# Kernel optimization log

Hardware: AMD Instinct MI355X
Metric: run time of the kernel (lower is better)

Reference implementation:

```python
import jax, jax.numpy as jnp
import numpy as np

SOFT_WINDOW_SIGMA = 4.0
QUERY_DIM = 512
B, T_DEC, T_ENC, D_V = 32, 2048, 2048, 512


def setup_inputs() -> dict:
    key = jax.random.key(0)
    kq, kk, kv = jax.random.split(key, 3)
    queries = jax.random.normal(kq, (B, T_DEC, QUERY_DIM), dtype=jnp.float32)
    keys = jax.random.normal(kk, (B, T_ENC, QUERY_DIM), dtype=jnp.float32)
    values = jax.random.normal(kv, (B, T_ENC, D_V), dtype=jnp.float32)
    return {"queries": queries, "keys": keys, "values": values}


def reference(queries, keys, values):
    # scores[b,i,j] = <q_i, k_j> ; [B, T_dec, T_enc]
    scale = 1.0 / np.sqrt(queries.shape[-1])
    scores = jnp.einsum('bid,bjd->bij', queries, keys)
    t_dec, t_enc = scores.shape[1], scores.shape[2]
    # soft window bias: (1 / (2*sigma^2)) * (i - (T_dec/T_enc) * j)
    i = jnp.arange(t_dec, dtype=jnp.float32)[:, None]
    j = jnp.arange(t_enc, dtype=jnp.float32)[None, :]
    soft_window = (1.0 / (2.0 * SOFT_WINDOW_SIGMA ** 2)) * (i - (t_dec / t_enc) * j)
    scores = jax.nn.softmax(scores * scale - soft_window, axis=2)
    summaries = jnp.einsum('bij,bjv->biv', scores, values)
    return (summaries, scores)
```

## Files before the change

kernel.cpp:

```cpp
#include <hip/hip_runtime.h>
#include <cstdint>
#include <cstddef>


#define NB 32
#define TD 2048
#define TE 2048
#define DQ 512
#define DV 512

static constexpr float SCALE = 0.04419417382415922f;
static constexpr float WBIAS = 0.03125f;

typedef __bf16 bf16x8 __attribute__((ext_vector_type(8)));
typedef float f32x4 __attribute__((ext_vector_type(4)));

__device__ __forceinline__ unsigned short f2bf(float x) {
  unsigned int u = __float_as_uint(x);
  u = (u + 0x7fffu + ((u >> 16) & 1u)) >> 16;
  return (unsigned short)u;
}

__device__ __forceinline__ void gload_lds16(const void* g, void* l) {
  __builtin_amdgcn_global_load_lds(
      (const __attribute__((address_space(1))) void*)g,
      (__attribute__((address_space(3))) void*)l, 16, 0, 0);
}

__global__ __launch_bounds__(256) void k_cvt(const float4* __restrict__ src,
                                             ushort4* __restrict__ dst) {
  int i = blockIdx.x * 256 + threadIdx.x;
  float4 v = src[i];
  dst[i] = make_ushort4(f2bf(v.x), f2bf(v.y), f2bf(v.z), f2bf(v.w));
}

__global__ __launch_bounds__(256) void k_vtrans(const float* __restrict__ V,
                                                unsigned short* __restrict__ Vt) {
  __shared__ float t[32 * 33];
  int b = blockIdx.z, j0 = blockIdx.y * 32, v0 = blockIdx.x * 32;
  int tid = threadIdx.x;
  int r = tid >> 3, c4 = (tid & 7) * 4;
  float4 in = *(const float4*)(V + ((size_t)b * TE + j0 + r) * DV + v0 + c4);
  t[r * 33 + c4 + 0] = in.x;
  t[r * 33 + c4 + 1] = in.y;
  t[r * 33 + c4 + 2] = in.z;
  t[r * 33 + c4 + 3] = in.w;
  __syncthreads();
  ushort4 o = make_ushort4(f2bf(t[(c4 + 0) * 33 + r]), f2bf(t[(c4 + 1) * 33 + r]),
                           f2bf(t[(c4 + 2) * 33 + r]), f2bf(t[(c4 + 3) * 33 + r]));
  *(ushort4*)(Vt + ((size_t)b * DV + v0 + r) * TE + j0 + c4) = o;
}

__global__ __launch_bounds__(256) void k_gemm1(const unsigned short* __restrict__ Qb,
                                               const unsigned short* __restrict__ Kb,
                                               float* __restrict__ Sc) {
  __shared__ __align__(16) unsigned short As[128 * 32];
  __shared__ __align__(16) unsigned short Bs[128 * 32];
  int bid = blockIdx.x;
  int xcd = bid & 7, slot = bid >> 3;
  int b = xcd + 8 * (slot >> 8);
  int tile = slot & 255;
  int it = tile >> 4, jt = tile & 15;

  int tid = threadIdx.x, w = tid >> 6, l = tid & 63;
  int lr = l >> 2, lc = (l & 3) * 8;
  int lm = l & 15, quad = l >> 4;
  int wr = (w >> 1) * 64, wc = (w & 1) * 64;

  const size_t qbase = ((size_t)b * TD + (size_t)it * 128) * DQ;
  const size_t kbase = ((size_t)b * TE + (size_t)jt * 128) * DQ;

  f32x4 acc[4][4];
  f32x4 zero = {0.f, 0.f, 0.f, 0.f};
  for (int mi = 0; mi < 4; ++mi)
    for (int ni = 0; ni < 4; ++ni) acc[mi][ni] = zero;

  for (int k0 = 0; k0 < DQ; k0 += 32) {
    for (int t = 0; t < 2; ++t) {
      int rg = (w * 2 + t) * 16;
      gload_lds16(Qb + qbase + (size_t)(rg + lr) * DQ + k0 + lc, &As[rg * 32]);
      gload_lds16(Kb + kbase + (size_t)(rg + lr) * DQ + k0 + lc, &Bs[rg * 32]);
    }
    __syncthreads();
    bf16x8 af[4], bfr[4];
    for (int mi = 0; mi < 4; ++mi)
      af[mi] = *(const bf16x8*)&As[(wr + mi * 16 + lm) * 32 + quad * 8];
    for (int ni = 0; ni < 4; ++ni)
      bfr[ni] = *(const bf16x8*)&Bs[(wc + ni * 16 + lm) * 32 + quad * 8];
    for (int mi = 0; mi < 4; ++mi)
      for (int ni = 0; ni < 4; ++ni)
        acc[mi][ni] = __builtin_amdgcn_mfma_f32_16x16x32_bf16(af[mi], bfr[ni],
                                                              acc[mi][ni], 0, 0, 0);
    __syncthreads();
  }

  for (int mi = 0; mi < 4; ++mi) {
    int ib = it * 128 + wr + mi * 16 + quad * 4;
    for (int ni = 0; ni < 4; ++ni) {
      int j = jt * 128 + wc + ni * 16 + lm;
      float* op = Sc + ((size_t)b * TD + ib) * TE + j;
      for (int r = 0; r < 4; ++r) {
        float lg = acc[mi][ni][r] * SCALE - (float)(ib + r - j) * WBIAS;
        op[(size_t)r * TE] = lg;
      }
    }
  }
}

__global__ __launch_bounds__(256) void k_softmax(float* __restrict__ Sc) {
  int w = threadIdx.x >> 6, l = threadIdx.x & 63;
  size_t row = (size_t)blockIdx.x * 4 + w;
  float4* p = (float4*)(Sc + row * TE);
  float4 v[8];
  float m = -3.0e38f;
  for (int t = 0; t < 8; ++t) {
    v[t] = p[l + 64 * t];
    m = fmaxf(m, fmaxf(fmaxf(v[t].x, v[t].y), fmaxf(v[t].z, v[t].w)));
  }
  for (int off = 32; off; off >>= 1) m = fmaxf(m, __shfl_xor(m, off));
  float s = 0.f;
  for (int t = 0; t < 8; ++t) {
    v[t].x = __expf(v[t].x - m);
    v[t].y = __expf(v[t].y - m);
    v[t].z = __expf(v[t].z - m);
    v[t].w = __expf(v[t].w - m);
    s += (v[t].x + v[t].y) + (v[t].z + v[t].w);
  }
  for (int off = 32; off; off >>= 1) s += __shfl_xor(s, off);
  float inv = 1.0f / s;
  for (int t = 0; t < 8; ++t) {
    v[t].x *= inv; v[t].y *= inv; v[t].z *= inv; v[t].w *= inv;
    p[l + 64 * t] = v[t];
  }
}

__global__ __launch_bounds__(256) void k_gemm2(const float* __restrict__ Sc,
                                               const unsigned short* __restrict__ Vt,
                                               float* __restrict__ O) {
  __shared__ __align__(16) unsigned short As[64 * 32];
  __shared__ __align__(16) unsigned short Bs[512 * 32];
  int bid = blockIdx.x;
  int xcd = bid & 7, slot = bid >> 3;
  int b = xcd + 8 * (slot >> 5);
  int it = slot & 31;
  int i0 = it * 64;

  int tid = threadIdx.x, w = tid >> 6, l = tid & 63;
  int lm = l & 15, quad = l >> 4;
  int lr = l >> 2, lc = (l & 3) * 8;
  int arow = tid >> 2, acg = (tid & 3) * 8;
  const float* ap = Sc + ((size_t)b * TD + i0 + arow) * TE + acg;

  f32x4 acc[4][8];
  f32x4 zero = {0.f, 0.f, 0.f, 0.f};
  for (int mi = 0; mi < 4; ++mi)
    for (int ni = 0; ni < 8; ++ni) acc[mi][ni] = zero;

  for (int k0 = 0; k0 < TE; k0 += 32) {
    float4 f0 = *(const float4*)(ap + k0);
    float4 f1 = *(const float4*)(ap + k0 + 4);
    *(ushort4*)&As[arow * 32 + acg] =
        make_ushort4(f2bf(f0.x), f2bf(f0.y), f2bf(f0.z), f2bf(f0.w));
    *(ushort4*)&As[arow * 32 + acg + 4] =
        make_ushort4(f2bf(f1.x), f2bf(f1.y), f2bf(f1.z), f2bf(f1.w));
    for (int q = 0; q < 8; ++q) {
      int vr = (w * 8 + q) * 16;
      gload_lds16(Vt + ((size_t)b * DV + vr + lr) * TE + k0 + lc, &Bs[vr * 32]);
    }
    __syncthreads();
    bf16x8 af[4];
    for (int mi = 0; mi < 4; ++mi)
      af[mi] = *(const bf16x8*)&As[(mi * 16 + lm) * 32 + quad * 8];
    for (int ni = 0; ni < 8; ++ni) {
      bf16x8 bfr = *(const bf16x8*)&Bs[(w * 128 + ni * 16 + lm) * 32 + quad * 8];
      for (int mi = 0; mi < 4; ++mi)
        acc[mi][ni] = __builtin_amdgcn_mfma_f32_16x16x32_bf16(af[mi], bfr,
                                                              acc[mi][ni], 0, 0, 0);
    }
    __syncthreads();
  }

  for (int mi = 0; mi < 4; ++mi) {
    int ib = i0 + mi * 16 + quad * 4;
    for (int ni = 0; ni < 8; ++ni) {
      int vc = w * 128 + ni * 16 + lm;
      float* op = O + ((size_t)b * TD + ib) * DV + vc;
      for (int r = 0; r < 4; ++r) op[(size_t)r * DV] = acc[mi][ni][r];
    }
  }
}

extern "C" void kernel_launch(void* const* d_in, const int* in_sizes, int n_in,
                              void* d_out, int out_size, void* d_ws, size_t ws_size,
                              hipStream_t stream) {
  const float* Q = (const float*)d_in[0];
  const float* K = (const float*)d_in[1];
  const float* V = (const float*)d_in[2];
  float* out = (float*)d_out;
  float* O = out;
  float* Sc = out + (size_t)NB * TD * DV;

  unsigned short* qb = (unsigned short*)d_ws;
  unsigned short* kb = qb + (size_t)NB * TD * DQ;
  unsigned short* vt = kb + (size_t)NB * TE * DQ;

  k_cvt<<<32768, 256, 0, stream>>>((const float4*)Q, (ushort4*)qb);
  k_cvt<<<32768, 256, 0, stream>>>((const float4*)K, (ushort4*)kb);
  k_vtrans<<<dim3(16, 64, 32), 256, 0, stream>>>(V, vt);
  k_gemm1<<<8192, 256, 0, stream>>>(qb, kb, Sc);
  k_softmax<<<16384, 256, 0, stream>>>(Sc);
  k_gemm2<<<1024, 256, 0, stream>>>(Sc, vt, O);
}
```

Baseline: 1.569 ms.

## Fuse softmax into GEMM epilogues via partial row max/sum statistics

The standalone softmax kernel is removed. The first GEMM epilogue now computes per-row partial max and sum-of-exp over each 64-column slice and stores them in the output buffer as scratch. The second GEMM merges these partials, normalizes the scores on the fly, writes the probabilities back and feeds them to the MFMA. This drops one full read pass over the large score matrix and one kernel launch. In exchange it adds extra exp work and cross-lane shuffles in both GEMMs and relies on the output buffer as temporary storage. The two Q/K conversion launches are also merged into a single kernel.

```diff
diff --git a/kernel.cpp b/kernel.cpp
--- a/kernel.cpp
+++ b/kernel.cpp
@@ -27,11 +27,21 @@
       (__attribute__((address_space(3))) void*)l, 16, 0, 0);
 }
 
-__global__ __launch_bounds__(256) void k_cvt(const float4* __restrict__ src,
-                                             ushort4* __restrict__ dst) {
-  int i = blockIdx.x * 256 + threadIdx.x;
-  float4 v = src[i];
-  dst[i] = make_ushort4(f2bf(v.x), f2bf(v.y), f2bf(v.z), f2bf(v.w));
+__global__ __launch_bounds__(256) void k_cvt2(const float4* __restrict__ Q,
+                                              ushort4* __restrict__ Qb,
+                                              const float4* __restrict__ K,
+                                              ushort4* __restrict__ Kb) {
+  int bid = blockIdx.x;
+  const float4* s;
+  ushort4* d;
+  int i;
+  if (bid < 32768) {
+    s = Q; d = Qb; i = bid * 256 + threadIdx.x;
+  } else {
+    s = K; d = Kb; i = (bid - 32768) * 256 + threadIdx.x;
+  }
+  float4 v = s[i];
+  d[i] = make_ushort4(f2bf(v.x), f2bf(v.y), f2bf(v.z), f2bf(v.w));
 }
 
 __global__ __launch_bounds__(256) void k_vtrans(const float* __restrict__ V,
@@ -53,7 +63,8 @@
 
 __global__ __launch_bounds__(256) void k_gemm1(const unsigned short* __restrict__ Qb,
                                                const unsigned short* __restrict__ Kb,
-                                               float* __restrict__ Sc) {
+                                               float* __restrict__ Sc,
+                                               float* __restrict__ St) {
   __shared__ __align__(16) unsigned short As[128 * 32];
   __shared__ __align__(16) unsigned short Bs[128 * 32];
   int bid = blockIdx.x;
@@ -96,47 +107,49 @@
 
   for (int mi = 0; mi < 4; ++mi) {
     int ib = it * 128 + wr + mi * 16 + quad * 4;
+    float lg[4][4];
+#pragma unroll
     for (int ni = 0; ni < 4; ++ni) {
       int j = jt * 128 + wc + ni * 16 + lm;
       float* op = Sc + ((size_t)b * TD + ib) * TE + j;
+#pragma unroll
       for (int r = 0; r < 4; ++r) {
-        float lg = acc[mi][ni][r] * SCALE - (float)(ib + r - j) * WBIAS;
-        op[(size_t)r * TE] = lg;
+        float v = acc[mi][ni][r] * SCALE - (float)(ib + r - j) * WBIAS;
+        lg[ni][r] = v;
+        op[(size_t)r * TE] = v;
       }
     }
-  }
-}
-
-__global__ __launch_bounds__(256) void k_softmax(float* __restrict__ Sc) {
-  int w = threadIdx.x >> 6, l = threadIdx.x & 63;
-  size_t row = (size_t)blockIdx.x * 4 + w;
-  float4* p = (float4*)(Sc + row * TE);
-  float4 v[8];
-  float m = -3.0e38f;
-  for (int t = 0; t < 8; ++t) {
-    v[t] = p[l + 64 * t];
-    m = fmaxf(m, fmaxf(fmaxf(v[t].x, v[t].y), fmaxf(v[t].z, v[t].w)));
-  }
-  for (int off = 32; off; off >>= 1) m = fmaxf(m, __shfl_xor(m, off));
-  float s = 0.f;
-  for (int t = 0; t < 8; ++t) {
-    v[t].x = __expf(v[t].x - m);
-    v[t].y = __expf(v[t].y - m);
-    v[t].z = __expf(v[t].z - m);
-    v[t].w = __expf(v[t].w - m);
-    s += (v[t].x + v[t].y) + (v[t].z + v[t].w);
-  }
-  for (int off = 32; off; off >>= 1) s += __shfl_xor(s, off);
-  float inv = 1.0f / s;
-  for (int t = 0; t < 8; ++t) {
-    v[t].x *= inv; v[t].y *= inv; v[t].z *= inv; v[t].w *= inv;
-    p[l + 64 * t] = v[t];
-  }
-}
-
-__global__ __launch_bounds__(256) void k_gemm2(const float* __restrict__ Sc,
+    float rmax[4], rsum[4];
+#pragma unroll
+    for (int r = 0; r < 4; ++r) {
+      float m = fmaxf(fmaxf(lg[0][r], lg[1][r]), fmaxf(lg[2][r], lg[3][r]));
+#pragma unroll
+      for (int off = 8; off; off >>= 1) m = fmaxf(m, __shfl_xor(m, off));
+      rmax[r] = m;
+    }
+#pragma unroll
+    for (int r = 0; r < 4; ++r) {
+      float s = __expf(lg[0][r] - rmax[r]) + __expf(lg[1][r] - rmax[r]) +
+                __expf(lg[2][r] - rmax[r]) + __expf(lg[3][r] - rmax[r]);
+#pragma unroll
+      for (int off = 8; off; off >>= 1) s += __shfl_xor(s, off);
+      rsum[r] = s;
+    }
+    if (lm == 0) {
+      int p = jt * 2 + (w & 1);
+#pragma unroll
+      for (int r = 0; r < 4; ++r) {
+        float* st = St + ((size_t)b * TD + ib + r) * DV;
+        st[p] = rmax[r];
+        st[32 + p] = rsum[r];
+      }
+    }
+  }
+}
+
+__global__ __launch_bounds__(256) void k_gemm2(float* Sc,
                                                const unsigned short* __restrict__ Vt,
-                                               float* __restrict__ O) {
+                                               float* O) {
   __shared__ __align__(16) unsigned short As[64 * 32];
   __shared__ __align__(16) unsigned short Bs[512 * 32];
   int bid = blockIdx.x;
@@ -149,7 +162,16 @@
   int lm = l & 15, quad = l >> 4;
   int lr = l >> 2, lc = (l & 3) * 8;
   int arow = tid >> 2, acg = (tid & 3) * 8;
-  const float* ap = Sc + ((size_t)b * TD + i0 + arow) * TE + acg;
+  float* scp = Sc + ((size_t)b * TD + i0 + arow) * TE + acg;
+
+  const float* st = O + ((size_t)b * TD + i0 + arow) * DV;
+  float M = -3.0e38f;
+#pragma unroll
+  for (int p = 0; p < 32; ++p) M = fmaxf(M, st[p]);
+  float S = 0.f;
+#pragma unroll
+  for (int p = 0; p < 32; ++p) S += st[32 + p] * __expf(st[p] - M);
+  float invS = 1.0f / S;
 
   f32x4 acc[4][8];
   f32x4 zero = {0.f, 0.f, 0.f, 0.f};
@@ -157,8 +179,18 @@
     for (int ni = 0; ni < 8; ++ni) acc[mi][ni] = zero;
 
   for (int k0 = 0; k0 < TE; k0 += 32) {
-    float4 f0 = *(const float4*)(ap + k0);
-    float4 f1 = *(const float4*)(ap + k0 + 4);
+    float4 f0 = *(const float4*)(scp + k0);
+    float4 f1 = *(const float4*)(scp + k0 + 4);
+    f0.x = __expf(f0.x - M) * invS;
+    f0.y = __expf(f0.y - M) * invS;
+    f0.z = __expf(f0.z - M) * invS;
+    f0.w = __expf(f0.w - M) * invS;
+    f1.x = __expf(f1.x - M) * invS;
+    f1.y = __expf(f1.y - M) * invS;
+    f1.z = __expf(f1.z - M) * invS;
+    f1.w = __expf(f1.w - M) * invS;
+    *(float4*)(scp + k0) = f0;
+    *(float4*)(scp + k0 + 4) = f1;
     *(ushort4*)&As[arow * 32 + acg] =
         make_ushort4(f2bf(f0.x), f2bf(f0.y), f2bf(f0.z), f2bf(f0.w));
     *(ushort4*)&As[arow * 32 + acg + 4] =
@@ -204,10 +236,9 @@
   unsigned short* kb = qb + (size_t)NB * TD * DQ;
   unsigned short* vt = kb + (size_t)NB * TE * DQ;
 
-  k_cvt<<<32768, 256, 0, stream>>>((const float4*)Q, (ushort4*)qb);
-  k_cvt<<<32768, 256, 0, stream>>>((const float4*)K, (ushort4*)kb);
+  k_cvt2<<<65536, 256, 0, stream>>>((const float4*)Q, (ushort4*)qb,
+                                    (const float4*)K, (ushort4*)kb);
   k_vtrans<<<dim3(16, 64, 32), 256, 0, stream>>>(V, vt);
-  k_gemm1<<<8192, 256, 0, stream>>>(qb, kb, Sc);
-  k_softmax<<<16384, 256, 0, stream>>>(Sc);
+  k_gemm1<<<8192, 256, 0, stream>>>(qb, kb, Sc, O);
   k_gemm2<<<1024, 256, 0, stream>>>(Sc, vt, O);
 }
```

Result: faster. 1.513 ms (-3.6%).
